# Performance work log

Measured on AMD Instinct MI355X. Metric: run time of the kernel, lower is better.

Reference implementation:

```python
import jax, jax.numpy as jnp
import numpy as np

B, S, D, H, E, K = 2, 2048, 1024, 4096, 8, 2


def setup_inputs() -> dict:
    key = jax.random.key(0)
    ks = jax.random.split(key, 5)
    x = jax.random.normal(ks[0], (B, S, D), dtype=jnp.float32)
    W = 0.02 * jax.random.normal(ks[1], (H, D), dtype=jnp.float32)
    bias = 0.02 * jax.random.normal(ks[2], (H,), dtype=jnp.float32)
    # alpha initialized near 1 (nn.Parameter(torch.ones(...)) + learned perturbation)
    alpha = 1.0 + 0.02 * jax.random.normal(ks[3], (E, D), dtype=jnp.float32)
    beta = 0.02 * jax.random.normal(ks[4], (E, D), dtype=jnp.float32)
    return {"x": x, "W": W, "bias": bias, "alpha": alpha, "beta": beta}


def reference(x, W, bias, alpha, beta):
    """MoEXLayer eval-mode forward (sparsity-aware routing + expert combine).

    x: [B,S,D], W: [H,D], bias: [H], alpha/beta: [E,D]. Returns [B,S,H].
    """
    E = alpha.shape[0]
    # --- Router: per-virtual-expert Gaussian pre-activation statistics ---
    # reconstructed_weight(alpha, beta) = W * alpha + beta  (column-wise affine)
    W_rec = W[None, :, :] * alpha[:, None, :] + beta[:, None, :]      # [E,H,D]
    mu_w = W_rec.mean(axis=1)                                          # [E,D]
    var_w = W_rec.var(axis=1)                                          # [E,D] (unbiased=False)
    mu_h = jnp.einsum('bsd,ed->bse', x, mu_w) + bias.mean()            # [B,S,E]
    sigma_h = jnp.sqrt(jnp.einsum('bsd,ed->bse', x * x, var_w) + 1e-8) # [B,S,E]
    router_logits = jax.lax.erf(mu_h / (jnp.sqrt(2.0) * sigma_h))      # [B,S,E]

    # --- Top-k routing: softmax over top-k logits, zeros elsewhere ---
    topk_vals, topk_idx = jax.lax.top_k(router_logits, K)              # [B,S,K]
    topk_w = jax.nn.softmax(topk_vals, axis=-1)                        # [B,S,K]
    router_weights = (jax.nn.one_hot(topk_idx, E, dtype=x.dtype)
                      * topk_w[..., None]).sum(axis=-2)                # [B,S,E]

    # --- Expert compute + combine (dispatch passes alpha only => beta=0) ---
    W_disp = W[None, :, :] * alpha[:, None, :]                         # [E,H,D]
    pre = jnp.einsum('bsd,ehd->bseh', x, W_disp) + bias                # [B,S,E,H]
    expert_out = jax.nn.relu(pre)
    out = jnp.einsum('bseh,bse->bsh', expert_out, router_weights)      # [B,S,H]
    return out
```

## Files before the change

### kernel.cpp

```cpp
#include <hip/hip_runtime.h>
#include <hip/hip_bf16.h>
#include <math.h>

#define DD 1024
#define HH 4096
#define EE 8
#define MTOK 4096
#define MROWS 8192

typedef __attribute__((ext_vector_type(8))) short bf16x8;
typedef __attribute__((ext_vector_type(4))) float f32x4;

__device__ __forceinline__ unsigned short f2bf(float x){
  __hip_bfloat16 h = __float2bfloat16(x);
  return *reinterpret_cast<unsigned short*>(&h);
}

__device__ __forceinline__ void gload16(const void* g, void* l){
  __builtin_amdgcn_global_load_lds((__attribute__((address_space(1))) void*)g,
                                   (__attribute__((address_space(3))) void*)l,
                                   16, 0, 0);
}

__global__ void cvtstats_kernel(const float4* __restrict__ W4, ushort4* __restrict__ Wb4,
                                float* __restrict__ pmean, float* __restrict__ pm2){
  int rc = blockIdx.x;
  int tid = threadIdx.x;
  double s0=0,s1=0,s2_=0,s3=0, q0=0,q1=0,q2=0,q3=0;
  for (int h = rc * 32; h < rc * 32 + 32; ++h){
    float4 w = W4[(size_t)h * 256 + tid];
    Wb4[(size_t)h * 256 + tid] = make_ushort4(f2bf(w.x), f2bf(w.y), f2bf(w.z), f2bf(w.w));
    s0 += w.x; q0 += (double)w.x * w.x;
    s1 += w.y; q1 += (double)w.y * w.y;
    s2_ += w.z; q2 += (double)w.z * w.z;
    s3 += w.w; q3 += (double)w.w * w.w;
  }
  int d0 = rc * DD + tid * 4;
  pmean[d0]   = (float)s0;  pm2[d0]   = (float)q0;
  pmean[d0+1] = (float)s1;  pm2[d0+1] = (float)q1;
  pmean[d0+2] = (float)s2_; pm2[d0+2] = (float)q2;
  pmean[d0+3] = (float)s3;  pm2[d0+3] = (float)q3;
}

__global__ void colstats_final_kernel(const float* __restrict__ pmean,
                                      const float* __restrict__ pm2,
                                      double* __restrict__ cmean, double* __restrict__ cvar){
  int d = blockIdx.x * 256 + threadIdx.x;
  double s = 0.0, s2 = 0.0;
  for (int c = 0; c < 128; ++c){ s += (double)pmean[c * DD + d]; s2 += (double)pm2[c * DD + d]; }
  double m = s / (double)HH;
  cmean[d] = m;
  cvar[d]  = s2 / (double)HH - m * m;
}

__global__ void biasmean_kernel(const float* __restrict__ bias, double* __restrict__ bmean){
  __shared__ double red[256];
  double s = 0.0;
  for (int h = threadIdx.x; h < HH; h += 256) s += (double)bias[h];
  red[threadIdx.x] = s;
  __syncthreads();
  for (int k = 128; k > 0; k >>= 1){
    if (threadIdx.x < k) red[threadIdx.x] += red[threadIdx.x + k];
    __syncthreads();
  }
  if (threadIdx.x == 0) *bmean = red[0] / (double)HH;
}

__global__ void muvw_kernel(const float* __restrict__ alpha, const float* __restrict__ beta,
                            const double* __restrict__ cmean, const double* __restrict__ cvar,
                            float* __restrict__ muw, float* __restrict__ vw){
  int i = blockIdx.x * 256 + threadIdx.x;
  int d = i & (DD - 1);
  double a = (double)alpha[i];
  muw[i] = (float)(a * cmean[d] + (double)beta[i]);
  vw[i]  = (float)(a * a * cvar[d]);
}

__global__ __launch_bounds__(256) void router_kernel(const float4* __restrict__ x4,
                                                     const float4* __restrict__ alpha4,
                                                     const float4* __restrict__ muw4,
                                                     const float4* __restrict__ vw4,
                                                     const double* __restrict__ bmeanp,
                                                     unsigned short* __restrict__ Xs,
                                                     float2* __restrict__ wpair){
  int wv = threadIdx.x >> 6, lane = threadIdx.x & 63;
  int t = blockIdx.x * 4 + wv;
  const float4* xt = x4 + (size_t)t * 256;

  float4 xv[4];
  double mu[EE], s2[EE];
  #pragma unroll
  for (int e = 0; e < EE; ++e){ mu[e] = 0.0; s2[e] = 0.0; }

  #pragma unroll
  for (int r = 0; r < 4; ++r){
    int c = lane + 64 * r;
    float4 xf = xt[c];
    xv[r] = xf;
    float x2x = xf.x * xf.x, x2y = xf.y * xf.y, x2z = xf.z * xf.z, x2w = xf.w * xf.w;
    #pragma unroll
    for (int e = 0; e < EE; ++e){
      float4 m4 = muw4[e * 256 + c];
      float4 v4 = vw4[e * 256 + c];
      mu[e] += (double)xf.x * m4.x + (double)xf.y * m4.y
             + (double)xf.z * m4.z + (double)xf.w * m4.w;
      s2[e] += (double)x2x * v4.x + (double)x2y * v4.y
             + (double)x2z * v4.z + (double)x2w * v4.w;
    }
  }

  #pragma unroll
  for (int off = 32; off > 0; off >>= 1){
    #pragma unroll
    for (int e = 0; e < EE; ++e){
      mu[e] += __shfl_xor(mu[e], off);
      s2[e] += __shfl_xor(s2[e], off);
    }
  }

  double bm = *bmeanp;
  double z[EE];
  #pragma unroll
  for (int e = 0; e < EE; ++e){
    double m = mu[e] + bm;
    double v = s2[e] + 1e-8;
    z[e] = m / sqrt(2.0 * v);
  }
  int e1 = 0;
  #pragma unroll
  for (int e = 1; e < EE; ++e) if (z[e] > z[e1]) e1 = e;
  int e2 = -1;
  #pragma unroll
  for (int e = 0; e < EE; ++e){
    if (e == e1) continue;
    if (e2 < 0 || z[e] > z[e2]) e2 = e;
  }
  double lg1 = erf(z[e1]), lg2 = erf(z[e2]);
  double ex = exp(lg2 - lg1);
  float w1 = (float)(1.0 / (1.0 + ex));
  float w2 = (float)(ex / (1.0 + ex));
  if (lane == 0) wpair[t] = make_float2(w1, w2);

  const float4* a1 = alpha4 + (size_t)e1 * 256;
  const float4* a2 = alpha4 + (size_t)e2 * 256;
  ushort4* X1 = (ushort4*)(Xs + (size_t)(2 * t) * DD);
  ushort4* X2 = (ushort4*)(Xs + (size_t)(2 * t + 1) * DD);
  #pragma unroll
  for (int r = 0; r < 4; ++r){
    int c = lane + 64 * r;
    float4 xf = xv[r];
    float4 av = a1[c];
    X1[c] = make_ushort4(f2bf(xf.x * av.x), f2bf(xf.y * av.y),
                         f2bf(xf.z * av.z), f2bf(xf.w * av.w));
    av = a2[c];
    X2[c] = make_ushort4(f2bf(xf.x * av.x), f2bf(xf.y * av.y),
                         f2bf(xf.z * av.z), f2bf(xf.w * av.w));
  }
}

#define BM 128
#define BN 128
#define BKT 64
#define NKT (DD / BKT)

__global__ __launch_bounds__(256, 2) void gemm_kernel(const unsigned short* __restrict__ Xs,
                                                      const unsigned short* __restrict__ Wb,
                                                      const float* __restrict__ bias,
                                                      const float2* __restrict__ wpair,
                                                      float* __restrict__ out){
  __shared__ __align__(16) unsigned short As[2 * 8192];
  __shared__ __align__(16) unsigned short Bs[2 * 8192];

  int tid = threadIdx.x, lane = tid & 63, wv = tid >> 6;
  int wr = wv >> 1, wc = wv & 1;
  int l15 = lane & 15;

  int bid = blockIdx.x;
  int ch = bid & 7, local = bid >> 3;
  int mtile = ch * 8 + (local & 7);
  int ntile = local >> 3;
  int bm0 = mtile * BM, bn0 = ntile * BN;

  int rl = lane >> 3;
  int cg = (lane & 7) ^ rl;
  const unsigned short* gA = Xs + (size_t)(bm0 + 32 * wv + rl) * DD + cg * 8;
  const unsigned short* gB = Wb + (size_t)(bn0 + 32 * wv + rl) * DD + cg * 8;

  int posr0 = (lane >> 4) ^ (l15 & 7);
  int posr1 = (4 + (lane >> 4)) ^ (l15 & 7);

  f32x4 acc[4][4] = {};

  auto stage = [&](int kt, int slot){
    int koff = kt * BKT;
    #pragma unroll
    for (int j = 0; j < 4; ++j){
      gload16(gA + (size_t)(8 * j) * DD + koff, (void*)(As + slot * 8192 + (4 * wv + j) * 512));
      gload16(gB + (size_t)(8 * j) * DD + koff, (void*)(Bs + slot * 8192 + (4 * wv + j) * 512));
    }
  };

  stage(0, 0);
  for (int t = 0; t < NKT; ++t){
    if (t < NKT - 1){
      stage(t + 1, (t + 1) & 1);
      asm volatile("s_waitcnt vmcnt(8)" ::: "memory");
    } else {
      asm volatile("s_waitcnt vmcnt(0)" ::: "memory");
    }
    __builtin_amdgcn_s_barrier();

    const unsigned short* Ab = As + (t & 1) * 8192;
    const unsigned short* Bb = Bs + (t & 1) * 8192;
    bf16x8 a0[4], a1[4], b0[4], b1[4];
    #pragma unroll
    for (int i = 0; i < 4; ++i){
      int ra = (wr * 64 + i * 16 + l15) * 64;
      a0[i] = *(const bf16x8*)(Ab + ra + posr0 * 8);
      a1[i] = *(const bf16x8*)(Ab + ra + posr1 * 8);
      int rb = (wc * 64 + i * 16 + l15) * 64;
      b0[i] = *(const bf16x8*)(Bb + rb + posr0 * 8);
      b1[i] = *(const bf16x8*)(Bb + rb + posr1 * 8);
    }

    __builtin_amdgcn_s_setprio(1);
    #pragma unroll
    for (int mi = 0; mi < 4; ++mi)
      #pragma unroll
      for (int ni = 0; ni < 4; ++ni){
        acc[mi][ni] = __builtin_amdgcn_mfma_f32_16x16x32_bf16(a0[mi], b0[ni], acc[mi][ni], 0, 0, 0);
        acc[mi][ni] = __builtin_amdgcn_mfma_f32_16x16x32_bf16(a1[mi], b1[ni], acc[mi][ni], 0, 0, 0);
      }
    __builtin_amdgcn_s_setprio(0);

    asm volatile("s_waitcnt lgkmcnt(0)" ::: "memory");
    __builtin_amdgcn_s_barrier();
  }

  #pragma unroll
  for (int mi = 0; mi < 4; ++mi){
    int rbase = wr * 64 + mi * 16 + ((lane >> 4) << 2);
    #pragma unroll
    for (int jp = 0; jp < 2; ++jp){
      int gm = bm0 + rbase + jp * 2;
      int t = gm >> 1;
      float2 w = wpair[t];
      #pragma unroll
      for (int ni = 0; ni < 4; ++ni){
        int gh = bn0 + wc * 64 + ni * 16 + l15;
        float bz = bias[gh];
        float v0 = acc[mi][ni][jp * 2]     + bz;
        float v1 = acc[mi][ni][jp * 2 + 1] + bz;
        out[(size_t)t * HH + gh] = w.x * fmaxf(v0, 0.f) + w.y * fmaxf(v1, 0.f);
      }
    }
  }
}

extern "C" void kernel_launch(void* const* d_in, const int* in_sizes, int n_in,
                              void* d_out, int out_size, void* d_ws, size_t ws_size,
                              hipStream_t stream) {
  const float* x     = (const float*)d_in[0];
  const float* W     = (const float*)d_in[1];
  const float* bias  = (const float*)d_in[2];
  const float* alpha = (const float*)d_in[3];
  const float* beta  = (const float*)d_in[4];
  float* out = (float*)d_out;

  char* ws = (char*)d_ws;
  unsigned short* Wb = (unsigned short*)ws;
  unsigned short* Xs = (unsigned short*)(ws + (8u << 20));
  float2* wpair      = (float2*)(ws + (24u << 20));
  double* cmean      = (double*)(ws + (24u << 20) + (64u << 10));
  double* cvar       = cmean + DD;
  double* bmean      = cvar + DD;
  float* pmean       = (float*)(ws + (24u << 20) + (128u << 10));
  float* pm2         = pmean + 128 * DD;
  float* muw         = (float*)(ws + (26u << 20));
  float* vw          = muw + EE * DD;

  cvtstats_kernel<<<128, 256, 0, stream>>>((const float4*)W, (ushort4*)Wb, pmean, pm2);
  colstats_final_kernel<<<4, 256, 0, stream>>>(pmean, pm2, cmean, cvar);
  biasmean_kernel<<<1, 256, 0, stream>>>(bias, bmean);
  muvw_kernel<<<32, 256, 0, stream>>>(alpha, beta, cmean, cvar, muw, vw);
  router_kernel<<<MTOK / 4, 256, 0, stream>>>((const float4*)x, (const float4*)alpha,
                                              (const float4*)muw, (const float4*)vw,
                                              bmean, Xs, wpair);
  gemm_kernel<<<(MROWS / BM) * (HH / BN), 256, 0, stream>>>(Xs, Wb, bias, wpair, out);
}
```

Before: 124.9 us.

## Enlarge GEMM tiles to 256x256 with 8 waves and phased LDS/MFMA schedule

Moves the expert GEMM from 128x128 tiles on 4 waves to 256x256 tiles on 8 waves. Each wave now owns a 128x64 output block, which raises reuse of every loaded operand. The K loop is split into four barrier-separated phases that interleave LDS fragment reads with MFMA bursts, and global-to-LDS loads are issued two tiles ahead. This gives 64 KB of LDS per block and 128 accumulator registers per lane, which may limit occupancy. The grid drops to 512 blocks, so wave quantisation across CUs is also a risk.

```diff
diff --git a/kernel.cpp b/kernel.cpp
--- a/kernel.cpp
+++ b/kernel.cpp
@@ -158,91 +158,112 @@
   }
 }
 
-#define BM 128
-#define BN 128
+#define BM 256
+#define BN 256
 #define BKT 64
 #define NKT (DD / BKT)
-
-__global__ __launch_bounds__(256, 2) void gemm_kernel(const unsigned short* __restrict__ Xs,
+#define ASLOT (BM * BKT)
+#define BSLOT (BN * BKT)
+
+__global__ __launch_bounds__(512, 2) void gemm_kernel(const unsigned short* __restrict__ Xs,
                                                       const unsigned short* __restrict__ Wb,
                                                       const float* __restrict__ bias,
                                                       const float2* __restrict__ wpair,
                                                       float* __restrict__ out){
-  __shared__ __align__(16) unsigned short As[2 * 8192];
-  __shared__ __align__(16) unsigned short Bs[2 * 8192];
+  __shared__ __align__(16) unsigned short As[2 * ASLOT];
+  __shared__ __align__(16) unsigned short Bs[2 * BSLOT];
 
   int tid = threadIdx.x, lane = tid & 63, wv = tid >> 6;
-  int wr = wv >> 1, wc = wv & 1;
+  int wr = wv >> 2, wc = wv & 3;
   int l15 = lane & 15;
 
   int bid = blockIdx.x;
   int ch = bid & 7, local = bid >> 3;
-  int mtile = ch * 8 + (local & 7);
-  int ntile = local >> 3;
+  int mtile = ch * 4 + (local & 3);
+  int ntile = local >> 2;
   int bm0 = mtile * BM, bn0 = ntile * BN;
 
-  int rl = lane >> 3;
-  int cg = (lane & 7) ^ rl;
-  const unsigned short* gA = Xs + (size_t)(bm0 + 32 * wv + rl) * DD + cg * 8;
-  const unsigned short* gB = Wb + (size_t)(bn0 + 32 * wv + rl) * DD + cg * 8;
-
-  int posr0 = (lane >> 4) ^ (l15 & 7);
-  int posr1 = (4 + (lane >> 4)) ^ (l15 & 7);
-
-  f32x4 acc[4][4] = {};
+  int sr = tid >> 3;
+  int sc = tid & 7;
+  int scg = sc ^ (sr & 7);
+  const unsigned short* gA = Xs + (size_t)(bm0 + sr) * DD + scg * 8;
+  const unsigned short* gB = Wb + (size_t)(bn0 + sr) * DD + scg * 8;
+  unsigned short* lA = As + tid * 8;
+  unsigned short* lB = Bs + tid * 8;
 
   auto stage = [&](int kt, int slot){
     int koff = kt * BKT;
     #pragma unroll
-    for (int j = 0; j < 4; ++j){
-      gload16(gA + (size_t)(8 * j) * DD + koff, (void*)(As + slot * 8192 + (4 * wv + j) * 512));
-      gload16(gB + (size_t)(8 * j) * DD + koff, (void*)(Bs + slot * 8192 + (4 * wv + j) * 512));
-    }
+    for (int j = 0; j < 4; ++j)
+      gload16(gA + (size_t)(64 * j) * DD + koff, lA + slot * ASLOT + j * (64 * BKT));
+    #pragma unroll
+    for (int j = 0; j < 4; ++j)
+      gload16(gB + (size_t)(64 * j) * DD + koff, lB + slot * BSLOT + j * (64 * BKT));
   };
 
+  int x7 = l15 & 7;
+  int chk0 = (lane >> 4) ^ x7;
+  int chk1 = (4 + (lane >> 4)) ^ x7;
+  const unsigned short* Arow = As + (wr * 128 + l15) * BKT;
+  const unsigned short* Brow = Bs + (wc * 64 + l15) * BKT;
+
+  f32x4 acc[8][4] = {};
+  bf16x8 afr[4], bfr[4];
+
   stage(0, 0);
-  for (int t = 0; t < NKT; ++t){
-    if (t < NKT - 1){
-      stage(t + 1, (t + 1) & 1);
-      asm volatile("s_waitcnt vmcnt(8)" ::: "memory");
-    } else {
-      asm volatile("s_waitcnt vmcnt(0)" ::: "memory");
-    }
-    __builtin_amdgcn_s_barrier();
-
-    const unsigned short* Ab = As + (t & 1) * 8192;
-    const unsigned short* Bb = Bs + (t & 1) * 8192;
-    bf16x8 a0[4], a1[4], b0[4], b1[4];
-    #pragma unroll
-    for (int i = 0; i < 4; ++i){
-      int ra = (wr * 64 + i * 16 + l15) * 64;
-      a0[i] = *(const bf16x8*)(Ab + ra + posr0 * 8);
-      a1[i] = *(const bf16x8*)(Ab + ra + posr1 * 8);
-      int rb = (wc * 64 + i * 16 + l15) * 64;
-      b0[i] = *(const bf16x8*)(Bb + rb + posr0 * 8);
-      b1[i] = *(const bf16x8*)(Bb + rb + posr1 * 8);
-    }
-
-    __builtin_amdgcn_s_setprio(1);
-    #pragma unroll
-    for (int mi = 0; mi < 4; ++mi)
-      #pragma unroll
-      for (int ni = 0; ni < 4; ++ni){
-        acc[mi][ni] = __builtin_amdgcn_mfma_f32_16x16x32_bf16(a0[mi], b0[ni], acc[mi][ni], 0, 0, 0);
-        acc[mi][ni] = __builtin_amdgcn_mfma_f32_16x16x32_bf16(a1[mi], b1[ni], acc[mi][ni], 0, 0, 0);
-      }
-    __builtin_amdgcn_s_setprio(0);
-
-    asm volatile("s_waitcnt lgkmcnt(0)" ::: "memory");
-    __builtin_amdgcn_s_barrier();
-  }
-
-  #pragma unroll
-  for (int mi = 0; mi < 4; ++mi){
-    int rbase = wr * 64 + mi * 16 + ((lane >> 4) << 2);
+  stage(1, 1);
+  asm volatile("s_waitcnt vmcnt(8)" ::: "memory");
+  __builtin_amdgcn_s_barrier();
+
+  #define PHASE(MH, CHK, READB)                                                  \
+    {                                                                            \
+      if (READB){                                                                \
+        _Pragma("unroll")                                                        \
+        for (int ni = 0; ni < 4; ++ni)                                           \
+          bfr[ni] = *(const bf16x8*)(Ab2 + ni * (16 * BKT) + (CHK) * 8);         \
+      }                                                                          \
+      _Pragma("unroll")                                                          \
+      for (int i = 0; i < 4; ++i)                                                \
+        afr[i] = *(const bf16x8*)(Ab1 + ((MH) * 4 + i) * (16 * BKT) + (CHK) * 8);\
+      __builtin_amdgcn_s_barrier();                                              \
+      asm volatile("s_waitcnt lgkmcnt(0)" ::: "memory");                         \
+      __builtin_amdgcn_sched_barrier(0);                                         \
+      __builtin_amdgcn_s_setprio(1);                                             \
+      _Pragma("unroll")                                                          \
+      for (int mi = 0; mi < 4; ++mi)                                             \
+        _Pragma("unroll")                                                        \
+        for (int ni = 0; ni < 4; ++ni)                                           \
+          acc[(MH) * 4 + mi][ni] =                                               \
+            __builtin_amdgcn_mfma_f32_16x16x32_bf16(afr[mi], bfr[ni],            \
+                                                    acc[(MH) * 4 + mi][ni], 0, 0, 0); \
+      __builtin_amdgcn_s_setprio(0);                                             \
+      __builtin_amdgcn_s_barrier();                                              \
+    }
+
+  #pragma unroll 1
+  for (int kt = 0; kt < NKT; ++kt){
+    int slot = kt & 1;
+    const unsigned short* Ab1 = Arow + slot * ASLOT;
+    const unsigned short* Ab2 = Brow + slot * BSLOT;
+    PHASE(0, chk0, 1)
+    PHASE(1, chk0, 0)
+    PHASE(0, chk1, 1)
+    PHASE(1, chk1, 0)
+    if (kt + 2 < NKT) stage(kt + 2, slot);
+    if (kt + 1 < NKT){
+      if (kt + 2 < NKT) asm volatile("s_waitcnt vmcnt(8)" ::: "memory");
+      else              asm volatile("s_waitcnt vmcnt(0)" ::: "memory");
+      __builtin_amdgcn_s_barrier();
+    }
+  }
+  #undef PHASE
+
+  #pragma unroll
+  for (int mi = 0; mi < 8; ++mi){
+    int rbase = bm0 + wr * 128 + mi * 16 + ((lane >> 4) << 2);
     #pragma unroll
     for (int jp = 0; jp < 2; ++jp){
-      int gm = bm0 + rbase + jp * 2;
+      int gm = rbase + jp * 2;
       int t = gm >> 1;
       float2 w = wpair[t];
       #pragma unroll
@@ -286,5 +307,5 @@
   router_kernel<<<MTOK / 4, 256, 0, stream>>>((const float4*)x, (const float4*)alpha,
                                               (const float4*)muw, (const float4*)vw,
                                               bmean, Xs, wpair);
-  gemm_kernel<<<(MROWS / BM) * (HH / BN), 256, 0, stream>>>(Xs, Wb, bias, wpair, out);
-}
+  gemm_kernel<<<(MROWS / BM) * (HH / BN), 512, 0, stream>>>(Xs, Wb, bias, wpair, out);
+}
```

New measurement: 125.3 us. Within noise of the previous version (+0.4%).
